# Kernel tuning notes

Measured on AMD Instinct MI355X. Metric: run time of the kernel, lower is better.

The kernel has to match this reference:

```python
import jax, jax.numpy as jnp
import numpy as np

# Standard NF4 lookup table (16 quantile values of a normal distribution)
NF4_TABLE = jnp.array([
    -1.0, -0.6961928009986877, -0.5250730514526367, -0.39491748809814453,
    -0.28444138169288635, -0.18477343022823334, -0.09105003625154495, 0.0,
    0.07958029955625534, 0.16093020141124725, 0.24611230194568634,
    0.33791524171829224, 0.44070982933044434, 0.5626170039176941,
    0.7229568362236023, 1.0], dtype=jnp.float32)
BLOCK = 64  # per-block quantization block size


def dequant_nf4(codes, scalers):
    """codes: int [out, in] values in [0,16); scalers: float [out*in/BLOCK]."""
    shape = codes.shape
    vals = NF4_TABLE[codes.reshape(-1, BLOCK)]  # [n_blocks, BLOCK]
    return (vals * scalers[:, None]).reshape(shape)


def setup_inputs() -> dict:
    key = jax.random.key(0)
    ks = jax.random.split(key, 7)
    D, H, T = 4096, 11008, 8192
    nb1 = H * D // BLOCK
    x = jax.random.normal(ks[0], (T, D), dtype=jnp.float32)
    w1_codes = jax.random.randint(ks[1], (H, D), 0, 16, dtype=jnp.int32)
    w1_scalers = jax.random.uniform(ks[2], (nb1,), dtype=jnp.float32) * 0.02
    w2_codes = jax.random.randint(ks[3], (H, D), 0, 16, dtype=jnp.int32)
    w2_scalers = jax.random.uniform(ks[4], (nb1,), dtype=jnp.float32) * 0.02
    w3_codes = jax.random.randint(ks[5], (D, H), 0, 16, dtype=jnp.int32)
    w3_scalers = jax.random.uniform(ks[6], (nb1,), dtype=jnp.float32) * 0.02
    return {"x": x, "w1_codes": w1_codes, "w1_scalers": w1_scalers,
            "w2_codes": w2_codes, "w2_scalers": w2_scalers,
            "w3_codes": w3_codes, "w3_scalers": w3_scalers}


def reference(x, w1_codes, w1_scalers, w2_codes, w2_scalers, w3_codes, w3_scalers):
    w1 = dequant_nf4(w1_codes, w1_scalers)  # [H, D]
    w2 = dequant_nf4(w2_codes, w2_scalers)  # [H, D]
    w3 = dequant_nf4(w3_codes, w3_scalers)  # [D, H]
    h = jax.nn.silu(x @ w1.T) * (x @ w2.T)  # [T, H]
    return h @ w3.T                          # [T, D]
```

## Files before the change

kernel.cpp:

```cpp
#include <hip/hip_runtime.h>
#include <hip/hip_bf16.h>

#define T_DIM 8192
#define D_DIM 4096
#define H_DIM 11008

typedef __attribute__((ext_vector_type(8))) __bf16 bf16x8;
typedef __attribute__((ext_vector_type(4))) float f32x4;

typedef __attribute__((address_space(1))) const void gvoid_t;
typedef __attribute__((address_space(3))) void lvoid_t;

__device__ __forceinline__ void async_lds16(const void* g, void* l) {
    __builtin_amdgcn_global_load_lds((gvoid_t*)g, (lvoid_t*)l, 16, 0, 0);
}

__device__ const float NF4_TAB[16] = {
    -1.0f, -0.6961928009986877f, -0.5250730514526367f, -0.39491748809814453f,
    -0.28444138169288635f, -0.18477343022823334f, -0.09105003625154495f, 0.0f,
    0.07958029955625534f, 0.16093020141124725f, 0.24611230194568634f,
    0.33791524171829224f, 0.44070982933044434f, 0.5626170039176941f,
    0.7229568362236023f, 1.0f};

__global__ void dequant_nf4_kernel(const int* __restrict__ codes,
                                   const float* __restrict__ scalers,
                                   __bf16* __restrict__ out, long n) {
    __shared__ float tbl[16];
    if (threadIdx.x < 16) tbl[threadIdx.x] = NF4_TAB[threadIdx.x];
    __syncthreads();
    long i = ((long)blockIdx.x * blockDim.x + threadIdx.x) * 8;
    if (i >= n) return;
    float s = scalers[i >> 6];
    const int4* cp = (const int4*)(codes + i);
    int4 c0 = cp[0], c1 = cp[1];
    bf16x8 v;
    v[0] = (__bf16)(tbl[c0.x] * s);
    v[1] = (__bf16)(tbl[c0.y] * s);
    v[2] = (__bf16)(tbl[c0.z] * s);
    v[3] = (__bf16)(tbl[c0.w] * s);
    v[4] = (__bf16)(tbl[c1.x] * s);
    v[5] = (__bf16)(tbl[c1.y] * s);
    v[6] = (__bf16)(tbl[c1.z] * s);
    v[7] = (__bf16)(tbl[c1.w] * s);
    *(bf16x8*)(out + i) = v;
}

__global__ void cvt_f32_bf16(const float* __restrict__ x, __bf16* __restrict__ out, long n) {
    long i = ((long)blockIdx.x * blockDim.x + threadIdx.x) * 8;
    if (i >= n) return;
    const float4* xp = (const float4*)(x + i);
    float4 f0 = xp[0], f1 = xp[1];
    bf16x8 v;
    v[0] = (__bf16)f0.x; v[1] = (__bf16)f0.y; v[2] = (__bf16)f0.z; v[3] = (__bf16)f0.w;
    v[4] = (__bf16)f1.x; v[5] = (__bf16)f1.y; v[6] = (__bf16)f1.z; v[7] = (__bf16)f1.w;
    *(bf16x8*)(out + i) = v;
}

template<int KD, int SILU, typename OutT>
__global__ __launch_bounds__(512, 2) void gemm_nt(
    const __bf16* __restrict__ A, const __bf16* __restrict__ B1,
    const __bf16* __restrict__ B2, OutT* __restrict__ Out, const int N)
{
    static_assert(KD % 128 == 0, "need an even number of K-tiles");
    __shared__ __bf16 lds[2 * 2 * 256 * 64];

    const int tid  = threadIdx.x;
    const int lane = tid & 63;
    const int wave = tid >> 6;
    const int wm = wave >> 2;
    const int wn = wave & 3;

    const int nwg  = gridDim.x * gridDim.y;
    const int bid0 = blockIdx.y * gridDim.x + blockIdx.x;
    const int bid  = (bid0 & 7) * (nwg >> 3) + (bid0 >> 3);
    const int bx = bid % gridDim.x;
    const int by = bid / gridDim.x;
    const long m0 = (long)by * 256;
    const long n0 = (long)bx * (SILU ? 128 : 256);

    const int sr = tid >> 3;
    const int sb = (tid & 7) ^ (sr & 7);
    const __bf16* Arow = A + (m0 + sr) * (long)KD + sb * 8;
    const __bf16* Brow;
    if (SILU) {
        const __bf16* matp = (sr & 16) ? B2 : B1;
        Brow = matp + (n0 + ((sr >> 5) << 4) + (sr & 15)) * (long)KD + sb * 8;
    } else {
        Brow = B1 + (n0 + sr) * (long)KD + sb * 8;
    }
    __bf16* dstA = &lds[(wave << 3) * 64];
    __bf16* dstB = dstA + 16384;

    const long BH = (SILU ? 64 : 128) * (long)KD;
    const long BA = (SILU ? 32 : 64) * (long)KD;

#define STAGE_A(BUF, H, KT) do { \
        const __bf16* s_ = Arow + (long)(H) * 128 * KD + (long)(KT) * 64; \
        __bf16* d_ = dstA + (BUF) * 32768 + (H) * 8192; \
        async_lds16(s_, d_); \
        async_lds16(s_ + 64 * (long)KD, d_ + 4096); \
    } while (0)
#define STAGE_B(BUF, H, KT) do { \
        const __bf16* s_ = Brow + (long)(H) * BH + (long)(KT) * 64; \
        __bf16* d_ = dstB + (BUF) * 32768 + (H) * 8192; \
        async_lds16(s_, d_); \
        async_lds16(s_ + BA, d_ + 4096); \
    } while (0)

    const int r15 = lane & 15;
    const int hi2 = lane >> 4;
    const int l7  = lane & 7;
    const int aOff = (wm * 128 + r15) * 64;
    const int bOff = 16384 + (wn * 64 + r15) * 64;

    auto rdA = [&](int buf, int m, int kk) -> bf16x8 {
        return *(const bf16x8*)&lds[buf * 32768 + aOff + m * 1024 +
                                    (((kk * 4 + hi2) ^ l7) << 3)];
    };
    auto rdB = [&](int buf, int n, int kk) -> bf16x8 {
        return *(const bf16x8*)&lds[buf * 32768 + bOff + n * 1024 +
                                    (((kk * 4 + hi2) ^ l7) << 3)];
    };

    f32x4 acc[8][4];
    const f32x4 z4 = {0.f, 0.f, 0.f, 0.f};
#pragma unroll
    for (int m = 0; m < 8; ++m)
#pragma unroll
        for (int n = 0; n < 4; ++n) acc[m][n] = z4;

    bf16x8 aF[8][2];
    bf16x8 bF[4][2];

#define LOAD_A4(BUF, MB) { _Pragma("unroll") for (int m_ = 0; m_ < 4; ++m_) { \
        aF[m_ + MB][0] = rdA(BUF, m_ + MB, 0); \
        aF[m_ + MB][1] = rdA(BUF, m_ + MB, 1); } }
#define LOAD_B2(BUF, NB) { _Pragma("unroll") for (int n_ = 0; n_ < 2; ++n_) { \
        bF[n_ + NB][0] = rdB(BUF, n_ + NB, 0); \
        bF[n_ + NB][1] = rdB(BUF, n_ + NB, 1); } }
#define QUAD(MB, NB) { _Pragma("unroll") for (int m_ = 0; m_ < 4; ++m_) { \
        _Pragma("unroll") for (int n_ = 0; n_ < 2; ++n_) { \
        acc[m_ + MB][n_ + NB] = __builtin_amdgcn_mfma_f32_16x16x32_bf16( \
            aF[m_ + MB][0], bF[n_ + NB][0], acc[m_ + MB][n_ + NB], 0, 0, 0); \
        acc[m_ + MB][n_ + NB] = __builtin_amdgcn_mfma_f32_16x16x32_bf16( \
            aF[m_ + MB][1], bF[n_ + NB][1], acc[m_ + MB][n_ + NB], 0, 0, 0); } } }
#define BAR()  __builtin_amdgcn_s_barrier()
#define LGK0() asm volatile("s_waitcnt lgkmcnt(0)" ::: "memory")
#define VM6()  asm volatile("s_waitcnt vmcnt(6)" ::: "memory")
#define PRIO1() __builtin_amdgcn_s_setprio(1)
#define PRIO0() __builtin_amdgcn_s_setprio(0)

#define TILE(BUF, T1, T2) \
    LOAD_A4(BUF, 0); LOAD_B2(BUF, 0); \
    STAGE_B(1 - (BUF), 1, T1); \
    BAR(); LGK0(); PRIO1(); QUAD(0, 0); PRIO0(); BAR(); \
    LOAD_A4(BUF, 4); LOAD_B2(BUF, 2); \
    BAR(); LGK0(); PRIO1(); QUAD(0, 2); PRIO0(); BAR(); \
    STAGE_A(BUF, 0, T2); STAGE_A(BUF, 1, T2); \
    PRIO1(); QUAD(4, 2); PRIO0(); \
    STAGE_B(BUF, 0, T2); \
    PRIO1(); QUAD(4, 0); PRIO0(); \
    VM6(); BAR();

    const int NT = KD / 64;

    STAGE_A(0, 0, 0); STAGE_A(0, 1, 0);
    STAGE_B(0, 0, 0); STAGE_B(0, 1, 0);
    STAGE_A(1, 0, 1); STAGE_A(1, 1, 1);
    STAGE_B(1, 0, 1);
    VM6();
    BAR();

#pragma unroll 1
    for (int t = 0; t < NT; t += 2) {
        const int t1 = t + 1;
        int t2 = t + 2; if (t2 >= NT) t2 -= NT;
        int t3 = t + 3; if (t3 >= NT) t3 -= NT;
        TILE(0, t1, t2);
        TILE(1, t2, t3);
    }
    asm volatile("s_waitcnt vmcnt(0)" ::: "memory");

    const int crow = hi2 * 4;
    if (SILU) {
#pragma unroll
        for (int m = 0; m < 8; ++m)
#pragma unroll
            for (int p = 0; p < 2; ++p)
#pragma unroll
                for (int r = 0; r < 4; ++r) {
                    const long row = m0 + wm * 128 + m * 16 + crow + r;
                    const long idx = row * (long)N + (n0 + wn * 32 + p * 16 + r15);
                    float a = acc[m][2 * p][r];
                    float b = acc[m][2 * p + 1][r];
                    float sg = 1.0f / (1.0f + __expf(-a));
                    Out[idx] = (OutT)(a * sg * b);
                }
    } else {
#pragma unroll
        for (int m = 0; m < 8; ++m)
#pragma unroll
            for (int n = 0; n < 4; ++n)
#pragma unroll
                for (int r = 0; r < 4; ++r) {
                    const long row = m0 + wm * 128 + m * 16 + crow + r;
                    const long idx = row * (long)N + (n0 + wn * 64 + n * 16 + r15);
                    Out[idx] = (OutT)acc[m][n][r];
                }
    }
#undef STAGE_A
#undef STAGE_B
#undef LOAD_A4
#undef LOAD_B2
#undef QUAD
#undef TILE
#undef BAR
#undef LGK0
#undef VM6
#undef PRIO1
#undef PRIO0
}

extern "C" void kernel_launch(void* const* d_in, const int* in_sizes, int n_in,
                              void* d_out, int out_size, void* d_ws, size_t ws_size,
                              hipStream_t stream) {
    const float* x   = (const float*)d_in[0];
    const int*   w1c = (const int*)d_in[1];
    const float* w1s = (const float*)d_in[2];
    const int*   w2c = (const int*)d_in[3];
    const float* w2s = (const float*)d_in[4];
    const int*   w3c = (const int*)d_in[5];
    const float* w3s = (const float*)d_in[6];
    float* out = (float*)d_out;

    char* ws = (char*)d_ws;
    __bf16* xb  = (__bf16*)ws;  ws += (size_t)T_DIM * D_DIM * 2;
    __bf16* w1b = (__bf16*)ws;  ws += (size_t)H_DIM * D_DIM * 2;
    __bf16* w2b = (__bf16*)ws;  ws += (size_t)H_DIM * D_DIM * 2;
    __bf16* w3b = (__bf16*)ws;  ws += (size_t)H_DIM * D_DIM * 2;
    __bf16* hb  = (__bf16*)ws;

    const long nx = (long)T_DIM * D_DIM;
    const long nw = (long)H_DIM * D_DIM;

    cvt_f32_bf16<<<(int)(nx / (256 * 8)), 256, 0, stream>>>(x, xb, nx);
    dequant_nf4_kernel<<<(int)(nw / (256 * 8)), 256, 0, stream>>>(w1c, w1s, w1b, nw);
    dequant_nf4_kernel<<<(int)(nw / (256 * 8)), 256, 0, stream>>>(w2c, w2s, w2b, nw);
    dequant_nf4_kernel<<<(int)(nw / (256 * 8)), 256, 0, stream>>>(w3c, w3s, w3b, nw);

    gemm_nt<D_DIM, 1, __bf16><<<dim3(H_DIM / 128, T_DIM / 256), 512, 0, stream>>>(
        xb, w1b, w2b, hb, H_DIM);
    gemm_nt<H_DIM, 0, float><<<dim3(D_DIM / 256, T_DIM / 256), 512, 0, stream>>>(
        hb, w3b, nullptr, out, D_DIM);
}
```

Measured before the change: 2.350 ms.

## Switch GEMM to 32x32x16 MFMA tiles and remap XCD block scheduling

```diff
diff --git a/kernel.cpp b/kernel.cpp
--- a/kernel.cpp
+++ b/kernel.cpp
@@ -7,6 +7,7 @@
 
 typedef __attribute__((ext_vector_type(8))) __bf16 bf16x8;
 typedef __attribute__((ext_vector_type(4))) float f32x4;
+typedef __attribute__((ext_vector_type(16))) float f32x16;
 
 typedef __attribute__((address_space(1))) const void gvoid_t;
 typedef __attribute__((address_space(3))) void lvoid_t;
@@ -72,9 +73,12 @@
 
     const int nwg  = gridDim.x * gridDim.y;
     const int bid0 = blockIdx.y * gridDim.x + blockIdx.x;
-    const int bid  = (bid0 & 7) * (nwg >> 3) + (bid0 >> 3);
-    const int bx = bid % gridDim.x;
-    const int by = bid / gridDim.x;
+    const int q    = nwg >> 3;
+    const int Rr   = q / gridDim.x;
+    const int xcd  = bid0 & 7;
+    const int j    = bid0 >> 3;
+    const int by   = xcd * Rr + (j % Rr);
+    const int bx   = j / Rr;
     const long m0 = (long)by * 256;
     const long n0 = (long)bx * (SILU ? 128 : 256);
 
@@ -83,8 +87,8 @@
     const __bf16* Arow = A + (m0 + sr) * (long)KD + sb * 8;
     const __bf16* Brow;
     if (SILU) {
-        const __bf16* matp = (sr & 16) ? B2 : B1;
-        Brow = matp + (n0 + ((sr >> 5) << 4) + (sr & 15)) * (long)KD + sb * 8;
+        const __bf16* matp = (sr & 32) ? B2 : B1;
+        Brow = matp + (n0 + (sr & 31)) * (long)KD + sb * 8;
     } else {
         Brow = B1 + (n0 + sr) * (long)KD + sb * 8;
     }
@@ -107,43 +111,42 @@
         async_lds16(s_ + BA, d_ + 4096); \
     } while (0)
 
-    const int r15 = lane & 15;
-    const int hi2 = lane >> 4;
+    const int l31 = lane & 31;
+    const int gh  = lane >> 5;
     const int l7  = lane & 7;
-    const int aOff = (wm * 128 + r15) * 64;
-    const int bOff = 16384 + (wn * 64 + r15) * 64;
-
-    auto rdA = [&](int buf, int m, int kk) -> bf16x8 {
-        return *(const bf16x8*)&lds[buf * 32768 + aOff + m * 1024 +
-                                    (((kk * 4 + hi2) ^ l7) << 3)];
+    const int aOff = (wm * 128 + l31) * 64;
+    const int bOff = 16384 + (wn * 64 + l31) * 64;
+
+    auto rdA = [&](int buf, int mt, int kk) -> bf16x8 {
+        return *(const bf16x8*)&lds[buf * 32768 + aOff + mt * 2048 +
+                                    (((kk * 2 + gh) ^ l7) << 3)];
     };
-    auto rdB = [&](int buf, int n, int kk) -> bf16x8 {
-        return *(const bf16x8*)&lds[buf * 32768 + bOff + n * 1024 +
-                                    (((kk * 4 + hi2) ^ l7) << 3)];
+    auto rdB = [&](int buf, int nt, int kk) -> bf16x8 {
+        return *(const bf16x8*)&lds[buf * 32768 + bOff + nt * 2048 +
+                                    (((kk * 2 + gh) ^ l7) << 3)];
     };
 
-    f32x4 acc[8][4];
-    const f32x4 z4 = {0.f, 0.f, 0.f, 0.f};
-#pragma unroll
-    for (int m = 0; m < 8; ++m)
-#pragma unroll
-        for (int n = 0; n < 4; ++n) acc[m][n] = z4;
-
-    bf16x8 aF[8][2];
-    bf16x8 bF[4][2];
-
-#define LOAD_A4(BUF, MB) { _Pragma("unroll") for (int m_ = 0; m_ < 4; ++m_) { \
-        aF[m_ + MB][0] = rdA(BUF, m_ + MB, 0); \
-        aF[m_ + MB][1] = rdA(BUF, m_ + MB, 1); } }
-#define LOAD_B2(BUF, NB) { _Pragma("unroll") for (int n_ = 0; n_ < 2; ++n_) { \
-        bF[n_ + NB][0] = rdB(BUF, n_ + NB, 0); \
-        bF[n_ + NB][1] = rdB(BUF, n_ + NB, 1); } }
-#define QUAD(MB, NB) { _Pragma("unroll") for (int m_ = 0; m_ < 4; ++m_) { \
-        _Pragma("unroll") for (int n_ = 0; n_ < 2; ++n_) { \
-        acc[m_ + MB][n_ + NB] = __builtin_amdgcn_mfma_f32_16x16x32_bf16( \
-            aF[m_ + MB][0], bF[n_ + NB][0], acc[m_ + MB][n_ + NB], 0, 0, 0); \
-        acc[m_ + MB][n_ + NB] = __builtin_amdgcn_mfma_f32_16x16x32_bf16( \
-            aF[m_ + MB][1], bF[n_ + NB][1], acc[m_ + MB][n_ + NB], 0, 0, 0); } } }
+    f32x16 acc[4][2];
+    const f32x16 z16 = {0.f,0.f,0.f,0.f,0.f,0.f,0.f,0.f,
+                        0.f,0.f,0.f,0.f,0.f,0.f,0.f,0.f};
+#pragma unroll
+    for (int m = 0; m < 4; ++m)
+#pragma unroll
+        for (int n = 0; n < 2; ++n) acc[m][n] = z16;
+
+    bf16x8 aF[4][4];
+    bf16x8 bF[2][4];
+
+#define LOAD_AB(BUF, P) { _Pragma("unroll") for (int c_ = 0; c_ < 2; ++c_) { \
+        const int kk_ = 2 * (P) + c_; \
+        _Pragma("unroll") for (int m_ = 0; m_ < 4; ++m_) \
+            aF[m_][kk_] = rdA(BUF, m_, kk_); \
+        _Pragma("unroll") for (int n_ = 0; n_ < 2; ++n_) \
+            bF[n_][kk_] = rdB(BUF, n_, kk_); } }
+#define MFMA8(KK) { _Pragma("unroll") for (int m_ = 0; m_ < 4; ++m_) \
+        _Pragma("unroll") for (int n_ = 0; n_ < 2; ++n_) \
+            acc[m_][n_] = __builtin_amdgcn_mfma_f32_32x32x16_bf16( \
+                aF[m_][(KK)], bF[n_][(KK)], acc[m_][n_], 0, 0, 0); }
 #define BAR()  __builtin_amdgcn_s_barrier()
 #define LGK0() asm volatile("s_waitcnt lgkmcnt(0)" ::: "memory")
 #define VM6()  asm volatile("s_waitcnt vmcnt(6)" ::: "memory")
@@ -151,15 +154,14 @@
 #define PRIO0() __builtin_amdgcn_s_setprio(0)
 
 #define TILE(BUF, T1, T2) \
-    LOAD_A4(BUF, 0); LOAD_B2(BUF, 0); \
+    LOAD_AB(BUF, 0); \
     STAGE_B(1 - (BUF), 1, T1); \
-    BAR(); LGK0(); PRIO1(); QUAD(0, 0); PRIO0(); BAR(); \
-    LOAD_A4(BUF, 4); LOAD_B2(BUF, 2); \
-    BAR(); LGK0(); PRIO1(); QUAD(0, 2); PRIO0(); BAR(); \
+    BAR(); LGK0(); PRIO1(); MFMA8(0); MFMA8(1); PRIO0(); BAR(); \
+    LOAD_AB(BUF, 1); \
+    BAR(); LGK0(); PRIO1(); MFMA8(2); PRIO0(); BAR(); \
     STAGE_A(BUF, 0, T2); STAGE_A(BUF, 1, T2); \
-    PRIO1(); QUAD(4, 2); PRIO0(); \
+    PRIO1(); MFMA8(3); PRIO0(); \
     STAGE_B(BUF, 0, T2); \
-    PRIO1(); QUAD(4, 0); PRIO0(); \
     VM6(); BAR();
 
     const int NT = KD / 64;
@@ -181,38 +183,34 @@
     }
     asm volatile("s_waitcnt vmcnt(0)" ::: "memory");
 
-    const int crow = hi2 * 4;
     if (SILU) {
 #pragma unroll
-        for (int m = 0; m < 8; ++m)
-#pragma unroll
-            for (int p = 0; p < 2; ++p)
-#pragma unroll
-                for (int r = 0; r < 4; ++r) {
-                    const long row = m0 + wm * 128 + m * 16 + crow + r;
-                    const long idx = row * (long)N + (n0 + wn * 32 + p * 16 + r15);
-                    float a = acc[m][2 * p][r];
-                    float b = acc[m][2 * p + 1][r];
-                    float sg = 1.0f / (1.0f + __expf(-a));
-                    Out[idx] = (OutT)(a * sg * b);
-                }
+        for (int mt = 0; mt < 4; ++mt)
+#pragma unroll
+            for (int r = 0; r < 16; ++r) {
+                const long row = m0 + wm * 128 + mt * 32 + (r & 3) + 8 * (r >> 2) + 4 * gh;
+                const long idx = row * (long)N + (n0 + wn * 32 + l31);
+                float a = acc[mt][0][r];
+                float b = acc[mt][1][r];
+                float sg = 1.0f / (1.0f + __expf(-a));
+                Out[idx] = (OutT)(a * sg * b);
+            }
     } else {
 #pragma unroll
-        for (int m = 0; m < 8; ++m)
-#pragma unroll
-            for (int n = 0; n < 4; ++n)
-#pragma unroll
-                for (int r = 0; r < 4; ++r) {
-                    const long row = m0 + wm * 128 + m * 16 + crow + r;
-                    const long idx = row * (long)N + (n0 + wn * 64 + n * 16 + r15);
-                    Out[idx] = (OutT)acc[m][n][r];
+        for (int mt = 0; mt < 4; ++mt)
+#pragma unroll
+            for (int nt = 0; nt < 2; ++nt)
+#pragma unroll
+                for (int r = 0; r < 16; ++r) {
+                    const long row = m0 + wm * 128 + mt * 32 + (r & 3) + 8 * (r >> 2) + 4 * gh;
+                    const long idx = row * (long)N + (n0 + wn * 64 + nt * 32 + l31);
+                    Out[idx] = (OutT)acc[mt][nt][r];
                 }
     }
 #undef STAGE_A
 #undef STAGE_B
-#undef LOAD_A4
-#undef LOAD_B2
-#undef QUAD
+#undef LOAD_AB
+#undef MFMA8
 #undef TILE
 #undef BAR
 #undef LGK0
```

New measurement: 2.711 ms. 15.4% more time.
